# Performance work log

Measured on AMD Instinct MI355X. Metric: run time of the kernel, lower is better.

Reference implementation:

```python
import jax, jax.numpy as jnp
import numpy as np

M = 16          # max number of instance ids (0 = background)
DELTA_AGG = 0.5
DELTA_DIS = 3.0


def setup_inputs() -> dict:
    key = jax.random.key(0)
    k1, k2 = jax.random.split(key)
    preds = jax.random.normal(k1, (8, 6, 640, 640), dtype=jnp.float32)
    targets = jax.random.randint(k2, (8, 2, 640, 640), 0, M).astype(jnp.int32)
    return {"preds": preds, "targets": targets}


def _seg_sum(vals, ids):
    # vals: [P] or [P, C], ids: [P] -> segment sums with M segments
    return jax.ops.segment_sum(vals, ids, num_segments=M)


def reference(preds, targets):
    N = preds.shape[0]
    sim = preds[:, 2:, :, :].reshape(N, 4, -1).transpose(0, 2, 1)  # N x P x 4
    text = targets[:, 0].reshape(N, -1)                            # N x P
    kern = targets[:, 1].reshape(N, -1)                            # N x P
    P = sim.shape[1]

    seg = jax.vmap(_seg_sum)
    ones = jnp.ones((N, P), sim.dtype)
    cnt_k = seg(ones, kern)                         # N x M kernel pixel counts
    cnt_t = seg(ones, text)                         # N x M text pixel counts
    G = seg(sim, kern) / jnp.maximum(cnt_k, 1.0)[..., None]  # N x M x 4, G_Ki means

    inst = jnp.arange(M)
    valid = (cnt_k > 0) & (cnt_t > 0) & (inst[None, :] >= 1)  # N x M (skip id 0)
    nv = jnp.sum(valid, axis=1)                                # N, number of valid instances

    # ---- aggregation loss: per text pixel, distance to its instance's kernel mean
    G_t = jnp.take_along_axis(G, text[..., None], axis=1)      # N x P x 4
    d = jnp.linalg.norm(sim - G_t, axis=-1) - DELTA_AGG        # N x P
    l = jnp.log(jnp.square(jnp.maximum(d, 0.0)) + 1.0)         # N x P
    l_mean = seg(l, text) / jnp.maximum(cnt_t, 1.0)            # N x M per-instance mean
    agg = jnp.sum(jnp.where(valid, l_mean, 0.0), axis=1) / jnp.maximum(nv, 1)

    # ---- discrimination loss: pairwise distances between valid kernel means
    pair = valid[:, :, None] & valid[:, None, :] & ~jnp.eye(M, dtype=bool)[None]
    sq = jnp.sum(jnp.square(G[:, :, None, :] - G[:, None, :, :]), axis=-1)  # N x M x M
    dist = jnp.sqrt(jnp.where(pair, sq, 1.0))
    lp = jnp.where(pair, jnp.log(jnp.square(jnp.maximum(DELTA_DIS - dist, 0.0)) + 1.0), 0.0)
    dis = jnp.where(nv > 1, 0.5 * jnp.sum(lp, axis=(1, 2)) / jnp.maximum(nv * (nv - 1), 1), 0.0)

    return agg.astype(jnp.float32), dis.astype(jnp.float32)
```

## Files before the change

kernel.cpp:

```cpp
#include <hip/hip_runtime.h>
#include <math.h>

#define NB 8
#define MSEG 16
#define PPIX (640*640)
#define PV4 (PPIX/4)
#define GRIDX 128
#define STRIDE (GRIDX*256)
#define FULLCOV (3*STRIDE)
#define DELTA_AGG 0.5f
#define DELTA_DIS 3.0f

typedef float v2f __attribute__((ext_vector_type(2)));

#define OFF_A1 0
#define OFF_A2 (NB*80)
#define WS_ZERO_FLOATS (NB*112)

__global__ __launch_bounds__(256, 3) void pass1_kernel(
    const float* __restrict__ preds, const int* __restrict__ targets,
    float* __restrict__ ws) {
  const int n = blockIdx.y, blk = blockIdx.x;
  const int tid = threadIdx.x, lane = tid & 63, w = tid >> 6;

  const float4* __restrict__ pc0 = (const float4*)(preds + ((size_t)n*6 + 2)*PPIX);
  const float4* __restrict__ pc1 = (const float4*)(preds + ((size_t)n*6 + 3)*PPIX);
  const float4* __restrict__ pc2 = (const float4*)(preds + ((size_t)n*6 + 4)*PPIX);
  const float4* __restrict__ pc3 = (const float4*)(preds + ((size_t)n*6 + 5)*PPIX);
  const int4*  __restrict__ kernv = (const int4*)(targets + ((size_t)n*2 + 1)*PPIX);

  v2f acc01[MSEG], acc23[MSEG];
  float cntk[MSEG];
#pragma unroll
  for (int m = 0; m < MSEG; ++m) {
    acc01[m] = (v2f){0.f, 0.f}; acc23[m] = (v2f){0.f, 0.f}; cntk[m] = 0.f;
  }

#define PIX1(K, A0, A1, A2, A3) do {                                \
    int k_ = (K);                                                   \
    v2f p01 = {(A0), (A1)}, p23 = {(A2), (A3)};                     \
    _Pragma("unroll")                                               \
    for (int m = 1; m < MSEG; ++m) {                                \
      float fk = (k_ == m) ? 1.0f : 0.0f;                           \
      v2f fk2 = {fk, fk};                                           \
      acc01[m] = __builtin_elementwise_fma(fk2, p01, acc01[m]);     \
      acc23[m] = __builtin_elementwise_fma(fk2, p23, acc23[m]);     \
      cntk[m] += fk;                                                \
    } } while (0)

#define GRP1(KK, VA, VB, VC, VD) do {                \
    PIX1((KK).x, (VA).x, (VB).x, (VC).x, (VD).x);    \
    PIX1((KK).y, (VA).y, (VB).y, (VC).y, (VD).y);    \
    PIX1((KK).z, (VA).z, (VB).z, (VC).z, (VD).z);    \
    PIX1((KK).w, (VA).w, (VB).w, (VC).w, (VD).w);    \
  } while (0)

  const int base = blk*256 + tid;
  int4 kc = kernv[base];
  float4 va = pc0[base], vb = pc1[base], vc = pc2[base], vd = pc3[base];
  {
    const int p = base + STRIDE;
    int4 kn = kernv[p];
    float4 an = pc0[p], bn = pc1[p], cn = pc2[p], dn = pc3[p];
    GRP1(kc, va, vb, vc, vd);
    kc = kn; va = an; vb = bn; vc = cn; vd = dn;
  }
  {
    const int p = base + 2*STRIDE;
    int4 kn = kernv[p];
    float4 an = pc0[p], bn = pc1[p], cn = pc2[p], dn = pc3[p];
    GRP1(kc, va, vb, vc, vd);
    kc = kn; va = an; vb = bn; vc = cn; vd = dn;
  }
  {
    int4 kr; float4 ar, br, cr, dr;
    const int pr = FULLCOV + blk*32 + (tid & 31);
    if (tid < 32) { kr = kernv[pr]; ar = pc0[pr]; br = pc1[pr]; cr = pc2[pr]; dr = pc3[pr]; }
    GRP1(kc, va, vb, vc, vd);
    if (tid < 32) GRP1(kr, ar, br, cr, dr);
  }
#undef GRP1
#undef PIX1

  float acc[80];
#pragma unroll
  for (int m = 0; m < MSEG; ++m) {
    acc[m]      = acc01[m].x;
    acc[16 + m] = acc01[m].y;
    acc[32 + m] = acc23[m].x;
    acc[48 + m] = acc23[m].y;
    acc[64 + m] = cntk[m];
  }

#pragma unroll
  for (int s = 0; s < 6; ++s) {
    const int dist = 32 >> s;
    const bool hi = (lane & dist) != 0;
#pragma unroll
    for (int v = 0; v < (32 >> s); ++v) {
      float keep = hi ? acc[v + (32 >> s)] : acc[v];
      float send = hi ? acc[v] : acc[v + (32 >> s)];
      acc[v] = keep + __shfl_xor(send, dist);
    }
  }
  float cn16[16];
#pragma unroll
  for (int m = 0; m < MSEG; ++m) cn16[m] = acc[64 + m];
#pragma unroll
  for (int s = 0; s < 4; ++s) {
    const int dist = 32 >> s;
    const int half = 8 >> s;
    const bool hi = (lane & dist) != 0;
#pragma unroll
    for (int v = 0; v < half; ++v) {
      float keep = hi ? cn16[v + half] : cn16[v];
      float send = hi ? cn16[v] : cn16[v + half];
      cn16[v] = keep + __shfl_xor(send, dist);
    }
  }
  float ckt = cn16[0];
  ckt += __shfl_xor(ckt, 2);
  ckt += __shfl_xor(ckt, 1);

  __shared__ float s_v[4][64];
  __shared__ float s_c[4][16];
  s_v[w][lane] = acc[0];
  if ((lane & 3) == 0) s_c[w][lane >> 2] = ckt;
  __syncthreads();

  if (tid < 64) {
    atomicAdd(&ws[OFF_A1 + n*80 + tid],
              s_v[0][tid] + s_v[1][tid] + s_v[2][tid] + s_v[3][tid]);
  } else if (tid < 80) {
    int i = tid - 64;
    atomicAdd(&ws[OFF_A1 + n*80 + tid],
              s_c[0][i] + s_c[1][i] + s_c[2][i] + s_c[3][i]);
  }
}

__global__ __launch_bounds__(256, 4) void pass2_kernel(
    const float* __restrict__ preds, const int* __restrict__ targets,
    float* __restrict__ ws) {
  const int n = blockIdx.y, blk = blockIdx.x;
  const int tid = threadIdx.x, lane = tid & 63, w = tid >> 6;

  const float4* __restrict__ pc0 = (const float4*)(preds + ((size_t)n*6 + 2)*PPIX);
  const float4* __restrict__ pc1 = (const float4*)(preds + ((size_t)n*6 + 3)*PPIX);
  const float4* __restrict__ pc2 = (const float4*)(preds + ((size_t)n*6 + 4)*PPIX);
  const float4* __restrict__ pc3 = (const float4*)(preds + ((size_t)n*6 + 5)*PPIX);
  const int4*  __restrict__ textv = (const int4*)(targets + (size_t)n*2*PPIX);

  const int base = blk*256 + tid;
  int4 tc = textv[base];
  float4 va = pc0[base], vb = pc1[base], vc = pc2[base], vd = pc3[base];

  __shared__ float s_raw[80];
  __shared__ float4 s_G[MSEG];
  if (tid < 80) s_raw[tid] = ws[OFF_A1 + n*80 + tid];
  __syncthreads();
  if (tid < 64) {
    int ch = tid >> 4, m = tid & 15;
    ((float*)&s_G[m])[ch] = s_raw[ch*16 + m] / fmaxf(s_raw[64 + m], 1.0f);
  }
  __syncthreads();

  v2f lc[MSEG];
#pragma unroll
  for (int m = 0; m < MSEG; ++m) lc[m] = (v2f){0.f, 0.f};

#define PIX2(T, A0, A1, A2, A3) do {                            \
    int t_ = (T);                                               \
    float4 gv = s_G[t_];                                        \
    float dx = (A0) - gv.x, dy = (A1) - gv.y;                   \
    float dz = (A2) - gv.z, dw = (A3) - gv.w;                   \
    float sq = fmaf(dx, dx, fmaf(dy, dy, fmaf(dz, dz, dw*dw))); \
    float dd = fmaxf(__fsqrt_rn(sq) - DELTA_AGG, 0.f);          \
    float l = __logf(fmaf(dd, dd, 1.f));                        \
    v2f l1 = {l, 1.0f};                                         \
    _Pragma("unroll")                                           \
    for (int m = 1; m < MSEG; ++m) {                            \
      float fk = (t_ == m) ? 1.0f : 0.0f;                       \
      v2f fk2 = {fk, fk};                                       \
      lc[m] = __builtin_elementwise_fma(fk2, l1, lc[m]);        \
    } } while (0)

#define GRP2(TT, VA, VB, VC, VD) do {                \
    PIX2((TT).x, (VA).x, (VB).x, (VC).x, (VD).x);    \
    PIX2((TT).y, (VA).y, (VB).y, (VC).y, (VD).y);    \
    PIX2((TT).z, (VA).z, (VB).z, (VC).z, (VD).z);    \
    PIX2((TT).w, (VA).w, (VB).w, (VC).w, (VD).w);    \
  } while (0)

  {
    const int p = base + STRIDE;
    int4 tn = textv[p];
    float4 an = pc0[p], bn = pc1[p], cn = pc2[p], dn = pc3[p];
    GRP2(tc, va, vb, vc, vd);
    tc = tn; va = an; vb = bn; vc = cn; vd = dn;
  }
  {
    const int p = base + 2*STRIDE;
    int4 tn = textv[p];
    float4 an = pc0[p], bn = pc1[p], cn = pc2[p], dn = pc3[p];
    GRP2(tc, va, vb, vc, vd);
    tc = tn; va = an; vb = bn; vc = cn; vd = dn;
  }
  {
    int4 tr; float4 ar, br, cr, dr;
    const int pr = FULLCOV + blk*32 + (tid & 31);
    if (tid < 32) { tr = textv[pr]; ar = pc0[pr]; br = pc1[pr]; cr = pc2[pr]; dr = pc3[pr]; }
    GRP2(tc, va, vb, vc, vd);
    if (tid < 32) GRP2(tr, ar, br, cr, dr);
  }
#undef GRP2
#undef PIX2

  float ls[MSEG], ct[MSEG];
#pragma unroll
  for (int m = 0; m < MSEG; ++m) { ls[m] = lc[m].x; ct[m] = lc[m].y; }

  float t0, t1;
#pragma unroll
  for (int s = 0; s < 4; ++s) {
    const int dist = 32 >> s; const int half = 8 >> s;
    const bool hi = (lane & dist) != 0;
#pragma unroll
    for (int v = 0; v < half; ++v) {
      float keep = hi ? ls[v + half] : ls[v];
      float send = hi ? ls[v] : ls[v + half];
      ls[v] = keep + __shfl_xor(send, dist);
    }
  }
  t0 = ls[0]; t0 += __shfl_xor(t0, 2); t0 += __shfl_xor(t0, 1);
#pragma unroll
  for (int s = 0; s < 4; ++s) {
    const int dist = 32 >> s; const int half = 8 >> s;
    const bool hi = (lane & dist) != 0;
#pragma unroll
    for (int v = 0; v < half; ++v) {
      float keep = hi ? ct[v + half] : ct[v];
      float send = hi ? ct[v] : ct[v + half];
      ct[v] = keep + __shfl_xor(send, dist);
    }
  }
  t1 = ct[0]; t1 += __shfl_xor(t1, 2); t1 += __shfl_xor(t1, 1);

  __shared__ float s_l[4][16];
  __shared__ float s_t[4][16];
  if ((lane & 3) == 0) { s_l[w][lane >> 2] = t0; s_t[w][lane >> 2] = t1; }
  __syncthreads();

  if (tid < 16)
    atomicAdd(&ws[OFF_A2 + n*32 + tid],
              s_l[0][tid] + s_l[1][tid] + s_l[2][tid] + s_l[3][tid]);
  else if (tid < 32) {
    int i = tid - 16;
    atomicAdd(&ws[OFF_A2 + n*32 + tid],
              s_t[0][i] + s_t[1][i] + s_t[2][i] + s_t[3][i]);
  }
}

__global__ __launch_bounds__(256) void finalize2_kernel(
    const float* __restrict__ ws, float* __restrict__ out) {
  const int n = blockIdx.x;
  const int tid = threadIdx.x;

  __shared__ float raw1[80];
  __shared__ float s2[32];
  __shared__ float sG[MSEG][4];
  __shared__ int   sval[MSEG];
  __shared__ int   snv;
  __shared__ float red[256];
  __shared__ float agg_sum;

  if (tid < 80) raw1[tid] = ws[OFF_A1 + n*80 + tid];
  else if (tid >= 96 && tid < 128) s2[tid - 96] = ws[OFF_A2 + n*32 + (tid - 96)];
  __syncthreads();
  if (tid < 64) {
    int ch = tid >> 4, m = tid & 15;
    sG[m][ch] = raw1[ch*16 + m] / fmaxf(raw1[64 + m], 1.0f);
  }
  if (tid < MSEG)
    sval[tid] = (tid >= 1) && (raw1[64 + tid] > 0.f) && (s2[16 + tid] > 0.f);
  __syncthreads();
  if (tid == 0) { int nv = 0; for (int m = 0; m < MSEG; m++) nv += sval[m]; snv = nv; }

  float av = 0.f;
  if (tid < MSEG && sval[tid]) av = s2[tid] / fmaxf(s2[16 + tid], 1.0f);
  red[tid] = av;
  __syncthreads();
  for (int s = 128; s > 0; s >>= 1) {
    if (tid < s) red[tid] += red[tid + s];
    __syncthreads();
  }
  if (tid == 0) agg_sum = red[0];
  __syncthreads();

  float lp = 0.f;
  {
    int i = tid >> 4, j = tid & 15;
    if (i != j && sval[i] && sval[j]) {
      float dx = sG[i][0] - sG[j][0];
      float dy = sG[i][1] - sG[j][1];
      float dz = sG[i][2] - sG[j][2];
      float dw = sG[i][3] - sG[j][3];
      float dist = sqrtf(dx*dx + dy*dy + dz*dz + dw*dw);
      float t = fmaxf(DELTA_DIS - dist, 0.f);
      lp = logf(t*t + 1.f);
    }
  }
  red[tid] = lp;
  __syncthreads();
  for (int s = 128; s > 0; s >>= 1) {
    if (tid < s) red[tid] += red[tid + s];
    __syncthreads();
  }
  if (tid == 0) {
    int nv = snv;
    out[n] = agg_sum / (float)(nv > 1 ? nv : 1);
    out[NB + n] = (nv > 1) ? 0.5f * red[0] / (float)(nv * (nv - 1)) : 0.f;
  }
}

extern "C" void kernel_launch(void* const* d_in, const int* in_sizes, int n_in,
                              void* d_out, int out_size, void* d_ws, size_t ws_size,
                              hipStream_t stream) {
  const float* preds   = (const float*)d_in[0];
  const int*   targets = (const int*)d_in[1];
  float* out = (float*)d_out;
  float* ws  = (float*)d_ws;

  hipMemsetAsync(d_ws, 0, WS_ZERO_FLOATS * sizeof(float), stream);

  dim3 grid(GRIDX, NB);
  pass1_kernel<<<grid, 256, 0, stream>>>(preds, targets, ws);
  pass2_kernel<<<grid, 256, 0, stream>>>(preds, targets, ws);
  finalize2_kernel<<<NB, 256, 0, stream>>>(ws, out);
}
```

Before: 54.76 us.

## Replace atomics with per-block partials and count segments via wave ballot

Float atomics into a zeroed workspace are replaced by per-block partial sums written to distinct slots, which pass2 and finalize then reduce. This removes the memset launch and makes results deterministic. Per-segment pixel counts now come from wave-level ballot plus popcount instead of per-lane float accumulators, which drops one shuffle-reduction tree and frees registers. Pass1's launch bounds rise to 4 waves per SIMD. In exchange, every pass2 block re-reads 80x128 partials, and the ballot adds scalar work inside the hot per-pixel loop.

```diff
diff --git a/kernel.cpp b/kernel.cpp
--- a/kernel.cpp
+++ b/kernel.cpp
@@ -13,11 +13,10 @@
 
 typedef float v2f __attribute__((ext_vector_type(2)));
 
-#define OFF_A1 0
-#define OFF_A2 (NB*80)
-#define WS_ZERO_FLOATS (NB*112)
-
-__global__ __launch_bounds__(256, 3) void pass1_kernel(
+#define OFF_P1 0
+#define OFF_P2 (NB*80*GRIDX)
+
+__global__ __launch_bounds__(256, 4) void pass1_kernel(
     const float* __restrict__ preds, const int* __restrict__ targets,
     float* __restrict__ ws) {
   const int n = blockIdx.y, blk = blockIdx.x;
@@ -30,10 +29,10 @@
   const int4*  __restrict__ kernv = (const int4*)(targets + ((size_t)n*2 + 1)*PPIX);
 
   v2f acc01[MSEG], acc23[MSEG];
-  float cntk[MSEG];
+  int ck[MSEG];
 #pragma unroll
   for (int m = 0; m < MSEG; ++m) {
-    acc01[m] = (v2f){0.f, 0.f}; acc23[m] = (v2f){0.f, 0.f}; cntk[m] = 0.f;
+    acc01[m] = (v2f){0.f, 0.f}; acc23[m] = (v2f){0.f, 0.f}; ck[m] = 0;
   }
 
 #define PIX1(K, A0, A1, A2, A3) do {                                \
@@ -41,11 +40,12 @@
     v2f p01 = {(A0), (A1)}, p23 = {(A2), (A3)};                     \
     _Pragma("unroll")                                               \
     for (int m = 1; m < MSEG; ++m) {                                \
-      float fk = (k_ == m) ? 1.0f : 0.0f;                           \
+      bool pk = (k_ == m);                                          \
+      ck[m] += __popcll(__ballot(pk));                              \
+      float fk = pk ? 1.0f : 0.0f;                                  \
       v2f fk2 = {fk, fk};                                           \
       acc01[m] = __builtin_elementwise_fma(fk2, p01, acc01[m]);     \
       acc23[m] = __builtin_elementwise_fma(fk2, p23, acc23[m]);     \
-      cntk[m] += fk;                                                \
     } } while (0)
 
 #define GRP1(KK, VA, VB, VC, VD) do {                \
@@ -82,16 +82,14 @@
 #undef GRP1
 #undef PIX1
 
-  float acc[80];
+  float acc[64];
 #pragma unroll
   for (int m = 0; m < MSEG; ++m) {
     acc[m]      = acc01[m].x;
     acc[16 + m] = acc01[m].y;
     acc[32 + m] = acc23[m].x;
     acc[48 + m] = acc23[m].y;
-    acc[64 + m] = cntk[m];
-  }
-
+  }
 #pragma unroll
   for (int s = 0; s < 6; ++s) {
     const int dist = 32 >> s;
@@ -103,38 +101,23 @@
       acc[v] = keep + __shfl_xor(send, dist);
     }
   }
-  float cn16[16];
-#pragma unroll
-  for (int m = 0; m < MSEG; ++m) cn16[m] = acc[64 + m];
-#pragma unroll
-  for (int s = 0; s < 4; ++s) {
-    const int dist = 32 >> s;
-    const int half = 8 >> s;
-    const bool hi = (lane & dist) != 0;
-#pragma unroll
-    for (int v = 0; v < half; ++v) {
-      float keep = hi ? cn16[v + half] : cn16[v];
-      float send = hi ? cn16[v] : cn16[v + half];
-      cn16[v] = keep + __shfl_xor(send, dist);
-    }
-  }
-  float ckt = cn16[0];
-  ckt += __shfl_xor(ckt, 2);
-  ckt += __shfl_xor(ckt, 1);
 
   __shared__ float s_v[4][64];
-  __shared__ float s_c[4][16];
+  __shared__ int   s_c[4][MSEG];
   s_v[w][lane] = acc[0];
-  if ((lane & 3) == 0) s_c[w][lane >> 2] = ckt;
+  if (lane == 0) {
+#pragma unroll
+    for (int m = 0; m < MSEG; ++m) s_c[w][m] = ck[m];
+  }
   __syncthreads();
 
   if (tid < 64) {
-    atomicAdd(&ws[OFF_A1 + n*80 + tid],
-              s_v[0][tid] + s_v[1][tid] + s_v[2][tid] + s_v[3][tid]);
+    ws[OFF_P1 + ((size_t)n*80 + tid)*GRIDX + blk] =
+        s_v[0][tid] + s_v[1][tid] + s_v[2][tid] + s_v[3][tid];
   } else if (tid < 80) {
     int i = tid - 64;
-    atomicAdd(&ws[OFF_A1 + n*80 + tid],
-              s_c[0][i] + s_c[1][i] + s_c[2][i] + s_c[3][i]);
+    ws[OFF_P1 + ((size_t)n*80 + tid)*GRIDX + blk] =
+        (float)(s_c[0][i] + s_c[1][i] + s_c[2][i] + s_c[3][i]);
   }
 }
 
@@ -156,17 +139,27 @@
 
   __shared__ float s_raw[80];
   __shared__ float4 s_G[MSEG];
-  if (tid < 80) s_raw[tid] = ws[OFF_A1 + n*80 + tid];
+  if (tid < 80) {
+    const float4* p4 = (const float4*)(ws + OFF_P1 + ((size_t)n*80 + tid)*GRIDX);
+    float s = 0.f;
+#pragma unroll
+    for (int i = 0; i < GRIDX/4; ++i) {
+      float4 v = p4[i];
+      s += (v.x + v.y) + (v.z + v.w);
+    }
+    s_raw[tid] = s;
+  }
   __syncthreads();
   if (tid < 64) {
     int ch = tid >> 4, m = tid & 15;
-    ((float*)&s_G[m])[ch] = s_raw[ch*16 + m] / fmaxf(s_raw[64 + m], 1.0f);
-  }
-  __syncthreads();
-
-  v2f lc[MSEG];
-#pragma unroll
-  for (int m = 0; m < MSEG; ++m) lc[m] = (v2f){0.f, 0.f};
+    ((float*)&s_G[m])[ch] = s_raw[tid] / fmaxf(s_raw[64 + m], 1.0f);
+  }
+  __syncthreads();
+
+  float ls[MSEG];
+  int   ct[MSEG];
+#pragma unroll
+  for (int m = 0; m < MSEG; ++m) { ls[m] = 0.f; ct[m] = 0; }
 
 #define PIX2(T, A0, A1, A2, A3) do {                            \
     int t_ = (T);                                               \
@@ -176,12 +169,11 @@
     float sq = fmaf(dx, dx, fmaf(dy, dy, fmaf(dz, dz, dw*dw))); \
     float dd = fmaxf(__fsqrt_rn(sq) - DELTA_AGG, 0.f);          \
     float l = __logf(fmaf(dd, dd, 1.f));                        \
-    v2f l1 = {l, 1.0f};                                         \
     _Pragma("unroll")                                           \
     for (int m = 1; m < MSEG; ++m) {                            \
-      float fk = (t_ == m) ? 1.0f : 0.0f;                       \
-      v2f fk2 = {fk, fk};                                       \
-      lc[m] = __builtin_elementwise_fma(fk2, l1, lc[m]);        \
+      bool pt = (t_ == m);                                      \
+      ct[m] += __popcll(__ballot(pt));                          \
+      ls[m] = fmaf(pt ? 1.0f : 0.0f, l, ls[m]);                 \
     } } while (0)
 
 #define GRP2(TT, VA, VB, VC, VD) do {                \
@@ -215,11 +207,6 @@
 #undef GRP2
 #undef PIX2
 
-  float ls[MSEG], ct[MSEG];
-#pragma unroll
-  for (int m = 0; m < MSEG; ++m) { ls[m] = lc[m].x; ct[m] = lc[m].y; }
-
-  float t0, t1;
 #pragma unroll
   for (int s = 0; s < 4; ++s) {
     const int dist = 32 >> s; const int half = 8 >> s;
@@ -231,32 +218,26 @@
       ls[v] = keep + __shfl_xor(send, dist);
     }
   }
-  t0 = ls[0]; t0 += __shfl_xor(t0, 2); t0 += __shfl_xor(t0, 1);
-#pragma unroll
-  for (int s = 0; s < 4; ++s) {
-    const int dist = 32 >> s; const int half = 8 >> s;
-    const bool hi = (lane & dist) != 0;
-#pragma unroll
-    for (int v = 0; v < half; ++v) {
-      float keep = hi ? ct[v + half] : ct[v];
-      float send = hi ? ct[v] : ct[v + half];
-      ct[v] = keep + __shfl_xor(send, dist);
-    }
-  }
-  t1 = ct[0]; t1 += __shfl_xor(t1, 2); t1 += __shfl_xor(t1, 1);
-
-  __shared__ float s_l[4][16];
-  __shared__ float s_t[4][16];
-  if ((lane & 3) == 0) { s_l[w][lane >> 2] = t0; s_t[w][lane >> 2] = t1; }
+  float t0 = ls[0];
+  t0 += __shfl_xor(t0, 2);
+  t0 += __shfl_xor(t0, 1);
+
+  __shared__ float s_l[4][MSEG];
+  __shared__ int   s_t[4][MSEG];
+  if ((lane & 3) == 0) s_l[w][lane >> 2] = t0;
+  if (lane == 0) {
+#pragma unroll
+    for (int m = 0; m < MSEG; ++m) s_t[w][m] = ct[m];
+  }
   __syncthreads();
 
   if (tid < 16)
-    atomicAdd(&ws[OFF_A2 + n*32 + tid],
-              s_l[0][tid] + s_l[1][tid] + s_l[2][tid] + s_l[3][tid]);
+    ws[OFF_P2 + ((size_t)n*32 + tid)*GRIDX + blk] =
+        s_l[0][tid] + s_l[1][tid] + s_l[2][tid] + s_l[3][tid];
   else if (tid < 32) {
     int i = tid - 16;
-    atomicAdd(&ws[OFF_A2 + n*32 + tid],
-              s_t[0][i] + s_t[1][i] + s_t[2][i] + s_t[3][i]);
+    ws[OFF_P2 + ((size_t)n*32 + tid)*GRIDX + blk] =
+        (float)(s_t[0][i] + s_t[1][i] + s_t[2][i] + s_t[3][i]);
   }
 }
 
@@ -273,8 +254,25 @@
   __shared__ float red[256];
   __shared__ float agg_sum;
 
-  if (tid < 80) raw1[tid] = ws[OFF_A1 + n*80 + tid];
-  else if (tid >= 96 && tid < 128) s2[tid - 96] = ws[OFF_A2 + n*32 + (tid - 96)];
+  if (tid < 80) {
+    const float4* p4 = (const float4*)(ws + OFF_P1 + ((size_t)n*80 + tid)*GRIDX);
+    float s = 0.f;
+#pragma unroll
+    for (int i = 0; i < GRIDX/4; ++i) {
+      float4 v = p4[i];
+      s += (v.x + v.y) + (v.z + v.w);
+    }
+    raw1[tid] = s;
+  } else if (tid >= 128 && tid < 160) {
+    const float4* p4 = (const float4*)(ws + OFF_P2 + ((size_t)n*32 + (tid - 128))*GRIDX);
+    float s = 0.f;
+#pragma unroll
+    for (int i = 0; i < GRIDX/4; ++i) {
+      float4 v = p4[i];
+      s += (v.x + v.y) + (v.z + v.w);
+    }
+    s2[tid - 128] = s;
+  }
   __syncthreads();
   if (tid < 64) {
     int ch = tid >> 4, m = tid & 15;
@@ -330,8 +328,6 @@
   float* out = (float*)d_out;
   float* ws  = (float*)d_ws;
 
-  hipMemsetAsync(d_ws, 0, WS_ZERO_FLOATS * sizeof(float), stream);
-
   dim3 grid(GRIDX, NB);
   pass1_kernel<<<grid, 256, 0, stream>>>(preds, targets, ws);
   pass2_kernel<<<grid, 256, 0, stream>>>(preds, targets, ws);
```

Measured after the change: 62.34 us. 1.14x slower.

## Fuse finalize into pass2 via last-block counter and raise pass1 occupancy

Applied to the files above, without the earlier changes.

Removes the separate finalize kernel launch. The last block per batch to finish pass2, detected with an atomic counter and thread fences, computes the aggregation and discrimination losses from the shared kernel means it already holds. It also raises pass1's launch-bounds minimum blocks from 3 to 4, which may limit registers and cause spills. The finalize step depends on correct fencing for visibility of the atomically accumulated sums.

```diff
diff --git a/kernel.cpp b/kernel.cpp
--- a/kernel.cpp
+++ b/kernel.cpp
@@ -15,9 +15,10 @@
 
 #define OFF_A1 0
 #define OFF_A2 (NB*80)
-#define WS_ZERO_FLOATS (NB*112)
-
-__global__ __launch_bounds__(256, 3) void pass1_kernel(
+#define OFF_CTR (NB*112)
+#define WS_ZERO_BYTES ((NB*112 + NB) * 4)
+
+__global__ __launch_bounds__(256, 4) void pass1_kernel(
     const float* __restrict__ preds, const int* __restrict__ targets,
     float* __restrict__ ws) {
   const int n = blockIdx.y, blk = blockIdx.x;
@@ -140,7 +141,7 @@
 
 __global__ __launch_bounds__(256, 4) void pass2_kernel(
     const float* __restrict__ preds, const int* __restrict__ targets,
-    float* __restrict__ ws) {
+    float* __restrict__ ws, int* __restrict__ ctr, float* __restrict__ out) {
   const int n = blockIdx.y, blk = blockIdx.x;
   const int tid = threadIdx.x, lane = tid & 63, w = tid >> 6;
 
@@ -160,7 +161,7 @@
   __syncthreads();
   if (tid < 64) {
     int ch = tid >> 4, m = tid & 15;
-    ((float*)&s_G[m])[ch] = s_raw[ch*16 + m] / fmaxf(s_raw[64 + m], 1.0f);
+    ((float*)&s_G[m])[ch] = s_raw[tid] / fmaxf(s_raw[64 + m], 1.0f);
   }
   __syncthreads();
 
@@ -258,30 +259,24 @@
     atomicAdd(&ws[OFF_A2 + n*32 + tid],
               s_t[0][i] + s_t[1][i] + s_t[2][i] + s_t[3][i]);
   }
-}
-
-__global__ __launch_bounds__(256) void finalize2_kernel(
-    const float* __restrict__ ws, float* __restrict__ out) {
-  const int n = blockIdx.x;
-  const int tid = threadIdx.x;
-
-  __shared__ float raw1[80];
+
+  __threadfence();
+  __shared__ int s_last;
+  if (tid == 0) s_last = (atomicAdd(&ctr[n], 1) == GRIDX - 1);
+  __syncthreads();
+  if (!s_last) return;
+  __threadfence();
+
   __shared__ float s2[32];
-  __shared__ float sG[MSEG][4];
   __shared__ int   sval[MSEG];
   __shared__ int   snv;
   __shared__ float red[256];
   __shared__ float agg_sum;
 
-  if (tid < 80) raw1[tid] = ws[OFF_A1 + n*80 + tid];
-  else if (tid >= 96 && tid < 128) s2[tid - 96] = ws[OFF_A2 + n*32 + (tid - 96)];
-  __syncthreads();
-  if (tid < 64) {
-    int ch = tid >> 4, m = tid & 15;
-    sG[m][ch] = raw1[ch*16 + m] / fmaxf(raw1[64 + m], 1.0f);
-  }
+  if (tid < 32) s2[tid] = ws[OFF_A2 + n*32 + tid];
+  __syncthreads();
   if (tid < MSEG)
-    sval[tid] = (tid >= 1) && (raw1[64 + tid] > 0.f) && (s2[16 + tid] > 0.f);
+    sval[tid] = (tid >= 1) && (s_raw[64 + tid] > 0.f) && (s2[16 + tid] > 0.f);
   __syncthreads();
   if (tid == 0) { int nv = 0; for (int m = 0; m < MSEG; m++) nv += sval[m]; snv = nv; }
 
@@ -300,10 +295,9 @@
   {
     int i = tid >> 4, j = tid & 15;
     if (i != j && sval[i] && sval[j]) {
-      float dx = sG[i][0] - sG[j][0];
-      float dy = sG[i][1] - sG[j][1];
-      float dz = sG[i][2] - sG[j][2];
-      float dw = sG[i][3] - sG[j][3];
+      float4 gi = s_G[i], gj = s_G[j];
+      float dx = gi.x - gj.x, dy = gi.y - gj.y;
+      float dz = gi.z - gj.z, dw = gi.w - gj.w;
       float dist = sqrtf(dx*dx + dy*dy + dz*dz + dw*dw);
       float t = fmaxf(DELTA_DIS - dist, 0.f);
       lp = logf(t*t + 1.f);
@@ -329,11 +323,11 @@
   const int*   targets = (const int*)d_in[1];
   float* out = (float*)d_out;
   float* ws  = (float*)d_ws;
-
-  hipMemsetAsync(d_ws, 0, WS_ZERO_FLOATS * sizeof(float), stream);
+  int*   ctr = ((int*)d_ws) + OFF_CTR;
+
+  hipMemsetAsync(d_ws, 0, WS_ZERO_BYTES, stream);
 
   dim3 grid(GRIDX, NB);
   pass1_kernel<<<grid, 256, 0, stream>>>(preds, targets, ws);
-  pass2_kernel<<<grid, 256, 0, stream>>>(preds, targets, ws);
-  finalize2_kernel<<<NB, 256, 0, stream>>>(ws, out);
+  pass2_kernel<<<grid, 256, 0, stream>>>(preds, targets, ws, ctr, out);
 }
```

Measured after the change: 115.4 us. 111% more time.
